# Optimization experiments

Hardware: AMD Instinct MI355X
Metric: run time of the kernel (lower is better)

Reference implementation:

```python
import jax, jax.numpy as jnp
import numpy as np

NUM_EXECUTORS = 50
NUM_DAG_FEATURES = 3
EMB_DAG = 16
EMB_GLOB = 16
HIDDEN = [64, 64, 32]
B = 60000            # number of jobs (one per env in the batched rollout)
NODES_PER_JOB = 10
NODE_FEAT = 5


def _init_mlp(key, dims):
    ws, bs = [], []
    for i in range(len(dims) - 1):
        key, k = jax.random.split(key)
        scale = 1.0 / np.sqrt(dims[i])
        ws.append(jax.random.uniform(k, (dims[i], dims[i + 1]), jnp.float32, -scale, scale))
        bs.append(jnp.zeros((dims[i + 1],), jnp.float32))
    return ws, bs


def setup_inputs() -> dict:
    rng = np.random.default_rng(0)
    n_nodes = B * NODES_PER_JOB
    # dag_batch.ptr: job i owns nodes [i*NODES_PER_JOB, (i+1)*NODES_PER_JOB)
    ptr = np.arange(B + 1, dtype=np.int64) * NODES_PER_JOB
    job_indices = rng.permutation(B).astype(np.int64)
    # ragged action counts per job (exec_mask is a prefix mask of length num_exec_acts[i])
    num_exec_acts = rng.integers(1, NUM_EXECUTORS + 1, size=B).astype(np.int64)
    n_sel = num_exec_acts[job_indices]
    T = int(n_sel.sum())
    # per-ragged-row executor index: concat([arange(n) for n in n_sel]), vectorized
    starts = np.cumsum(n_sel) - n_sel
    exec_act_idx = (np.arange(T, dtype=np.int64) - np.repeat(starts, n_sel)).astype(np.int64)

    key = jax.random.key(0)
    k_x, k_hd, k_hg, k_mlp = jax.random.split(key, 4)
    x = jax.random.normal(k_x, (n_nodes, NODE_FEAT), jnp.float32)
    h_dag = jax.random.normal(k_hd, (B, EMB_DAG), jnp.float32)
    h_glob = jax.random.normal(k_hg, (B, EMB_GLOB), jnp.float32)

    in_dim = NUM_DAG_FEATURES + EMB_DAG + EMB_GLOB + 1  # 36
    ws, bs = _init_mlp(k_mlp, [in_dim] + HIDDEN + [1])

    return {
        "x": x,
        "h_dag": h_dag,
        "h_glob": h_glob,
        "ptr": jnp.asarray(ptr),
        "job_indices": jnp.asarray(job_indices),
        "num_exec_acts": jnp.asarray(num_exec_acts),
        "exec_act_idx": jnp.asarray(exec_act_idx),
        "W1": ws[0], "b1": bs[0],
        "W2": ws[1], "b2": bs[1],
        "W3": ws[2], "b3": bs[2],
        "W4": ws[3], "b4": bs[3],
    }


def reference(x, h_dag, h_glob, ptr, job_indices, num_exec_acts, exec_act_idx,
              W1, b1, W2, b2, W3, b3, W4, b4):
    T = exec_act_idx.shape[0]                       # total ragged action rows (static)
    J = job_indices.shape[0]
    # masked gather: dag features at each dag's start node, then select jobs
    x_dag = x[ptr[:-1], :NUM_DAG_FEATURES][job_indices]        # [J, 3]
    h_dag_sel = h_dag[job_indices]                              # [J, 16]
    x_h_dag = jnp.concatenate([x_dag, h_dag_sel], axis=1)       # [J, 19]
    # variable repeat_interleave -> gather by repeated row index
    n_sel = num_exec_acts[job_indices]
    rpt = jnp.repeat(jnp.arange(J), n_sel, total_repeat_length=T)
    x_h_rpt = x_h_dag[rpt]                                      # [T, 19]
    h_glob_rpt = h_glob[rpt]                                    # [T, 16]
    # exec action feature: k / num_executors for the k-th valid executor
    exec_actions = (exec_act_idx.astype(x.dtype) / NUM_EXECUTORS)[:, None]  # [T, 1]
    h = jnp.concatenate([x_h_rpt, h_glob_rpt, exec_actions], axis=1)        # [T, 36]
    h = jax.nn.relu(h @ W1 + b1)
    h = jax.nn.relu(h @ W2 + b2)
    h = jax.nn.relu(h @ W3 + b3)
    scores = (h @ W4 + b4).squeeze(-1)                          # [T]
    return scores
```

## Files before the change

kernel.cpp:

```cpp
#include <hip/hip_runtime.h>

#define TPB 256

using half8  = __attribute__((ext_vector_type(8))) _Float16;
using fp16x2 = __attribute__((ext_vector_type(2))) __fp16;
using f32x4  = __attribute__((ext_vector_type(4))) float;

static __device__ __forceinline__ unsigned pkrtz(float a, float b) {
    fp16x2 h = __builtin_amdgcn_cvt_pkrtz(a, b);
    return __builtin_bit_cast(unsigned, h);
}
template <int CTRL>
static __device__ __forceinline__ float dppmov(float x) {
    return __int_as_float(__builtin_amdgcn_mov_dpp(__float_as_int(x), CTRL, 0xF, 0xF, true));
}
#define DPP_SWAP 0xB1

__global__ __launch_bounds__(TPB) void k_prep(const float* __restrict__ x,
                                              const float* __restrict__ h_dag,
                                              const float* __restrict__ h_glob,
                                              const int* __restrict__ ptr,
                                              const int* __restrict__ job_indices,
                                              const int* __restrict__ num_exec_acts,
                                              int J, int nb,
                                              float* __restrict__ s_tab,
                                              int* __restrict__ bsum, int* __restrict__ jsv,
                                              const float* __restrict__ W1,
                                              const float* __restrict__ b1,
                                              const float* __restrict__ W2,
                                              const float* __restrict__ b2,
                                              const float* __restrict__ W3,
                                              const float* __restrict__ b3,
                                              const float* __restrict__ W4,
                                              uint4* __restrict__ wfrag,
                                              float4* __restrict__ bfrag)
{
    if (blockIdx.x == (unsigned)nb) {
        if (threadIdx.x < 64) {
            int lane = threadIdx.x;
            int n = lane & 15, q = lane >> 4;
#pragma unroll
            for (int nt = 0; nt < 4; nt++) {
#pragma unroll
                for (int s = 0; s < 2; s++) {
                    half8 w2f;
#pragma unroll
                    for (int jj = 0; jj < 8; jj++) {
                        int ks = s * 32 + q * 8 + jj;
                        w2f[jj] = (_Float16)W2[ks * 64 + nt * 16 + n];
                    }
                    wfrag[(8 + nt * 2 + s) * 64 + lane] = __builtin_bit_cast(uint4, w2f);
                }
            }
#pragma unroll
            for (int nt = 0; nt < 2; nt++) {
#pragma unroll
                for (int s = 0; s < 2; s++) {
                    half8 w3f;
#pragma unroll
                    for (int jj = 0; jj < 8; jj++) {
                        int ks = s * 32 + q * 8 + jj;
                        w3f[jj] = (_Float16)W3[ks * 32 + nt * 16 + n];
                    }
                    wfrag[(16 + nt * 2 + s) * 64 + lane] = __builtin_bit_cast(uint4, w3f);
                }
            }
            bfrag[1 * 64 + lane] = make_float4(b2[n], b2[16 + n], b2[32 + n], b2[48 + n]);
            bfrag[2 * 64 + lane] = make_float4(b3[n], b3[16 + n], W4[n], W4[16 + n]);
        }
        return;
    }

    __shared__ int sc[TPB];
    int j = blockIdx.x * TPB + threadIdx.x;
    int v = 0;
    if (j < J) {
        int ji   = job_indices[j];
        v        = num_exec_acts[ji];
        int node = ptr[ji];
        float f[35];
        f[0] = x[node * 5 + 0];
        f[1] = x[node * 5 + 1];
        f[2] = x[node * 5 + 2];
        float4 hd[4], hg[4];
#pragma unroll
        for (int c4 = 0; c4 < 4; c4++) hd[c4] = *(const float4*)(h_dag + (size_t)ji * 16 + 4 * c4);
#pragma unroll
        for (int c4 = 0; c4 < 4; c4++) hg[c4] = *(const float4*)(h_glob + (size_t)j * 16 + 4 * c4);
#pragma unroll
        for (int c4 = 0; c4 < 4; c4++) {
            f[3 + 4 * c4 + 0]  = hd[c4].x; f[3 + 4 * c4 + 1]  = hd[c4].y;
            f[3 + 4 * c4 + 2]  = hd[c4].z; f[3 + 4 * c4 + 3]  = hd[c4].w;
            f[19 + 4 * c4 + 0] = hg[c4].x; f[19 + 4 * c4 + 1] = hg[c4].y;
            f[19 + 4 * c4 + 2] = hg[c4].z; f[19 + 4 * c4 + 3] = hg[c4].w;
        }
        float acc[64];
#pragma unroll
        for (int d4 = 0; d4 < 16; d4++) {
            float4 b = *(const float4*)(b1 + 4 * d4);
            acc[4 * d4 + 0] = b.x; acc[4 * d4 + 1] = b.y;
            acc[4 * d4 + 2] = b.z; acc[4 * d4 + 3] = b.w;
        }
#pragma unroll
        for (int c = 0; c < 35; c++) {
            float fc = f[c];
#pragma unroll
            for (int d4 = 0; d4 < 16; d4++) {
                float4 w = *(const float4*)(W1 + c * 64 + 4 * d4);
                acc[4 * d4 + 0] += fc * w.x; acc[4 * d4 + 1] += fc * w.y;
                acc[4 * d4 + 2] += fc * w.z; acc[4 * d4 + 3] += fc * w.w;
            }
        }
        float4* sd = (float4*)(s_tab + (size_t)j * 64);
#pragma unroll
        for (int d4 = 0; d4 < 16; d4++)
            sd[d4] = make_float4(acc[4 * d4], acc[4 * d4 + 1], acc[4 * d4 + 2], acc[4 * d4 + 3]);
    }
    sc[threadIdx.x] = v;
    __syncthreads();
    for (int d = 1; d < TPB; d <<= 1) {
        int add = (threadIdx.x >= d) ? sc[threadIdx.x - d] : 0;
        __syncthreads();
        sc[threadIdx.x] += add;
        __syncthreads();
    }
    if (j < J) jsv[j] = ((sc[threadIdx.x] - v) << 6) | v;
    if (threadIdx.x == TPB - 1) bsum[blockIdx.x] = sc[TPB - 1];
}

__global__ __launch_bounds__(TPB) void k_mlp_mfma(const float* __restrict__ s_tab,
                                                  const float* __restrict__ W1,
                                                  const int* __restrict__ jsv,
                                                  const int* __restrict__ bsum,
                                                  const uint4* __restrict__ wfrag,
                                                  const float4* __restrict__ bfrag,
                                                  const float* __restrict__ b4,
                                                  float* __restrict__ out,
                                                  int T, int J, int nb, int numTiles, int chunk)
{
    __shared__ __align__(16) char smem[4 * 4096];
    __shared__ int boffs[TPB];
    __shared__ int swin[4][64];
    __shared__ int srow[4][64];
    const int tid  = threadIdx.x;
    const int lane = tid & 63;
    const int wv   = tid >> 6;
    const int n    = lane & 15;
    const int q    = lane >> 4;
    char* slab = smem + wv * 4096;

    {
        int v = (tid < nb) ? bsum[tid] : 0;
        boffs[tid] = v;
        __syncthreads();
        for (int d = 1; d < TPB; d <<= 1) {
            int add = (tid >= d) ? boffs[tid - d] : 0;
            __syncthreads();
            boffs[tid] += add;
            __syncthreads();
        }
        int ex = boffs[tid] - v;
        __syncthreads();
        boffs[tid] = ex;
        __syncthreads();
    }

    half8 bw2[4][2], bw3[2][2];
#pragma unroll
    for (int nt = 0; nt < 4; nt++)
#pragma unroll
        for (int s = 0; s < 2; s++)
            bw2[nt][s] = __builtin_bit_cast(half8, wfrag[(8 + nt * 2 + s) * 64 + lane]);
#pragma unroll
    for (int nt = 0; nt < 2; nt++)
#pragma unroll
        for (int s = 0; s < 2; s++)
            bw3[nt][s] = __builtin_bit_cast(half8, wfrag[(16 + nt * 2 + s) * 64 + lane]);

    float4 bf2 = bfrag[1 * 64 + lane];
    float4 bf3 = bfrag[2 * 64 + lane];
    float bb2[4] = {bf2.x, bf2.y, bf2.z, bf2.w};
    float bb3[2] = {bf3.x, bf3.y};
    const float w4a = bf3.z, w4b = bf3.w;
    const float b4v = b4[0];
    const int   swr = (n >> 1) & 7;
    const int   odd = n & 1;

    float w36[16];
    {
        const float* wp = W1 + 35 * 64 + q * 8;
        float4 wa0 = *(const float4*)(wp);
        float4 wa1 = *(const float4*)(wp + 4);
        float4 wb0 = *(const float4*)(wp + 32);
        float4 wb1 = *(const float4*)(wp + 36);
        w36[0]=wa0.x; w36[1]=wa0.y; w36[2]=wa0.z; w36[3]=wa0.w;
        w36[4]=wa1.x; w36[5]=wa1.y; w36[6]=wa1.z; w36[7]=wa1.w;
        w36[8]=wb0.x; w36[9]=wb0.y; w36[10]=wb0.z; w36[11]=wb0.w;
        w36[12]=wb1.x; w36[13]=wb1.y; w36[14]=wb1.z; w36[15]=wb1.w;
    }

    const int t0 = blockIdx.x * chunk;
    const int t1 = (t0 + chunk < numTiles) ? (t0 + chunk) : numTiles;
    const int R  = (t1 - t0) * 32;
    const int r0 = t0 * 128 + wv * R;
    int rend = r0 + R;
    if (rend > T) rend = T;

    if (r0 < rend) {
        int j_lo;
        {
            int lo = 0, hi = nb - 1;
            while (lo < hi) {
                int mid = (lo + hi + 1) >> 1;
                if (boffs[mid] <= r0) lo = mid; else hi = mid - 1;
            }
            j_lo = lo << 8;
        }
        int sreg    = 0;
        int win_top = 0x80000000;

        half8 a2[2][2];

        auto build_a2 = [&](int mtbase) {
#pragma unroll
            for (int m = 0; m < 2; m++) {
                int u   = srow[wv][16 * (mtbase + m) + n];
                int job = j_lo + (u >> 8);
                if (job > J - 1) job = J - 1;
                float e = (float)(u & 255) * 0.02f;
                const float* sp = s_tab + (size_t)job * 64 + q * 8;
                float4 s0 = *(const float4*)(sp);
                float4 s1 = *(const float4*)(sp + 4);
                float4 s2 = *(const float4*)(sp + 32);
                float4 s3 = *(const float4*)(sp + 36);
                float h[16];
                h[0]  = fmaxf(s0.x + e * w36[0],  0.0f); h[1]  = fmaxf(s0.y + e * w36[1],  0.0f);
                h[2]  = fmaxf(s0.z + e * w36[2],  0.0f); h[3]  = fmaxf(s0.w + e * w36[3],  0.0f);
                h[4]  = fmaxf(s1.x + e * w36[4],  0.0f); h[5]  = fmaxf(s1.y + e * w36[5],  0.0f);
                h[6]  = fmaxf(s1.z + e * w36[6],  0.0f); h[7]  = fmaxf(s1.w + e * w36[7],  0.0f);
                h[8]  = fmaxf(s2.x + e * w36[8],  0.0f); h[9]  = fmaxf(s2.y + e * w36[9],  0.0f);
                h[10] = fmaxf(s2.z + e * w36[10], 0.0f); h[11] = fmaxf(s2.w + e * w36[11], 0.0f);
                h[12] = fmaxf(s3.x + e * w36[12], 0.0f); h[13] = fmaxf(s3.y + e * w36[13], 0.0f);
                h[14] = fmaxf(s3.z + e * w36[14], 0.0f); h[15] = fmaxf(s3.w + e * w36[15], 0.0f);
                a2[m][0] = __builtin_bit_cast(half8, make_uint4(pkrtz(h[0], h[1]),  pkrtz(h[2], h[3]),
                                                                pkrtz(h[4], h[5]),  pkrtz(h[6], h[7])));
                a2[m][1] = __builtin_bit_cast(half8, make_uint4(pkrtz(h[8], h[9]),  pkrtz(h[10], h[11]),
                                                                pkrtz(h[12], h[13]), pkrtz(h[14], h[15])));
            }
        };

        auto stage_L2r = [&]() {
#pragma unroll
            for (int mt = 0; mt < 2; mt++) {
                f32x4 acc[4];
#pragma unroll
                for (int nt = 0; nt < 4; nt++) { f32x4 c; c[0]=c[1]=c[2]=c[3]=bb2[nt]; acc[nt]=c; }
#pragma unroll
                for (int s = 0; s < 2; s++) {
#pragma unroll
                    for (int nt = 0; nt < 4; nt++)
                        acc[nt] = __builtin_amdgcn_mfma_f32_16x16x32_f16(a2[mt][s], bw2[nt][s], acc[nt], 0, 0, 0);
                }
                unsigned* sl = (unsigned*)slab;
#pragma unroll
                for (int nt = 0; nt < 4; nt++) {
                    float v0 = fmaxf(acc[nt][0], 0.0f), v1 = fmaxf(acc[nt][1], 0.0f);
                    float v2 = fmaxf(acc[nt][2], 0.0f), v3 = fmaxf(acc[nt][3], 0.0f);
                    float t0_ = dppmov<DPP_SWAP>(v0), t1_ = dppmov<DPP_SWAP>(v1);
                    float t2_ = dppmov<DPP_SWAP>(v2), t3_ = dppmov<DPP_SWAP>(v3);
                    unsigned u0 = pkrtz(odd ? t2_ : v0, odd ? v2 : t0_);
                    unsigned u1 = pkrtz(odd ? t3_ : v1, odd ? v3 : t1_);
                    int rowA = 16 * mt + 4 * q + (odd ? 2 : 0);
                    int c    = 2 * nt + (n >> 3);
                    int a0   = (rowA * 8 + (c ^ ((rowA >> 1) & 7))) * 4 + ((n >> 1) & 3);
                    sl[a0] = u0; sl[a0 + 32] = u1;
                }
            }
        };

        auto stage_L34 = [&](int rbb) {
#pragma unroll
            for (int mt = 0; mt < 2; mt++) {
                const int M0 = 16 * mt;
                f32x4 acc[2];
#pragma unroll
                for (int nt = 0; nt < 2; nt++) { f32x4 c; c[0]=c[1]=c[2]=c[3]=bb3[nt]; acc[nt]=c; }
#pragma unroll
                for (int s = 0; s < 2; s++) {
                    half8 a = *(const half8*)(slab + ((M0 + n) * 8 + ((s * 4 + q) ^ swr)) * 16);
#pragma unroll
                    for (int nt = 0; nt < 2; nt++)
                        acc[nt] = __builtin_amdgcn_mfma_f32_16x16x32_f16(a, bw3[nt][s], acc[nt], 0, 0, 0);
                }
                f32x4 red;
#pragma unroll
                for (int r = 0; r < 4; r++)
                    red[r] = fmaxf(acc[0][r], 0.0f) * w4a + fmaxf(acc[1][r], 0.0f) * w4b;
#pragma unroll
                for (int r = 0; r < 4; r++) {
                    red[r] += dppmov<0x121>(red[r]);
                    red[r] += dppmov<0x122>(red[r]);
                    red[r] += dppmov<0x124>(red[r]);
                    red[r] += dppmov<0x128>(red[r]);
                }
                int t = rbb + M0 + q * 4 + n;
                float val = (n == 0) ? red[0] : (n == 1) ? red[1] : (n == 2) ? red[2] : red[3];
                if (n < 4 && t < T) out[t] = val + b4v;
            }
        };

        for (int rb = r0; rb < rend; rb += 64) {
            if (win_top <= rb + 63) {
                for (;;) {
                    int jj = j_lo + lane;
                    sreg = (jj < J) ? (boffs[jj >> 8] + (jsv[jj] >> 6)) : 0x7fffffff;
                    unsigned long long m = __ballot(sreg <= rb);
                    int adv = 63 - __builtin_clzll(m);
                    j_lo += adv;
                    if (adv == 0) break;
                }
                swin[wv][lane] = sreg;
                win_top = __shfl(sreg, 63);
            }

            {
                int rt = rb + lane;
                const int* sw = swin[wv];
                int lj = 0;
#pragma unroll
                for (int stp = 32; stp; stp >>= 1) {
                    int c2 = lj + stp;
                    if (c2 < 64 && sw[c2] <= rt) lj = c2;
                }
                srow[wv][lane] = (lj << 8) | (rt - sw[lj]);
            }

            build_a2(0);
            stage_L2r();
            stage_L34(rb);
            if (rb + 32 < rend) {
                build_a2(2);
                stage_L2r();
                stage_L34(rb + 32);
            }
        }
    }
}

extern "C" void kernel_launch(void* const* d_in, const int* in_sizes, int n_in,
                              void* d_out, int out_size, void* d_ws, size_t ws_size,
                              hipStream_t stream)
{
    const float* x             = (const float*)d_in[0];
    const float* h_dag         = (const float*)d_in[1];
    const float* h_glob        = (const float*)d_in[2];
    const int*   ptr           = (const int*)d_in[3];
    const int*   job_indices   = (const int*)d_in[4];
    const int*   num_exec_acts = (const int*)d_in[5];
    const float* W1 = (const float*)d_in[7];
    const float* b1 = (const float*)d_in[8];
    const float* W2 = (const float*)d_in[9];
    const float* b2 = (const float*)d_in[10];
    const float* W3 = (const float*)d_in[11];
    const float* b3 = (const float*)d_in[12];
    const float* W4 = (const float*)d_in[13];
    const float* b4 = (const float*)d_in[14];
    float* out = (float*)d_out;

    int J  = in_sizes[4];
    int T  = in_sizes[6];
    int nb = (J + TPB - 1) / TPB;

    char* wsp = (char*)d_ws;
    int* bsum = (int*)wsp;
    wsp += (((size_t)nb * 4) + 255) / 256 * 256;
    int* jsv = (int*)wsp;
    wsp += (((size_t)J * 4) + 255) / 256 * 256;
    uint4* wfrag = (uint4*)wsp;
    wsp += 20 * 64 * 16;
    float4* bfrag = (float4*)wsp;
    wsp += 3 * 64 * 16;
    float* s_tab = (float*)wsp;

    k_prep<<<nb + 1, TPB, 0, stream>>>(x, h_dag, h_glob, ptr, job_indices, num_exec_acts,
                                       J, nb, s_tab, bsum, jsv,
                                       W1, b1, W2, b2, W3, b3, W4, wfrag, bfrag);

    int numTiles = (T + 127) / 128;
    int grid = numTiles < 1280 ? numTiles : 1280;
    int chunk = (numTiles + grid - 1) / grid;
    grid = (numTiles + chunk - 1) / chunk;
    k_mlp_mfma<<<grid, TPB, 0, stream>>>(s_tab, W1, jsv, bsum, wfrag, bfrag, b4,
                                         out, T, J, nb, numTiles, chunk);
}
```

Before: 171.7 us.

## Store per-job layer-1 table in fp16 quarters and split prep across column blocks

The per-job layer-1 pre-activation table is now stored as fp16 in four 16-column quarter planes, and the prep kernel launches four times as many blocks, each computing one quarter of the 64 outputs. The MLP kernel gathers these halved rows and applies the executor-feature term and ReLU with packed fp16 math instead of fp32 plus conversion. The aim is to halve the gather traffic in the main kernel, cut per-thread register use in prep, and raise prep parallelism. The MLP grid cap is also raised. The cost is extra fp16 rounding in the layer-1 activations and redundant input loads across the four prep quarters.

```diff
diff --git a/kernel.cpp b/kernel.cpp
--- a/kernel.cpp
+++ b/kernel.cpp
@@ -4,11 +4,16 @@
 
 using half8  = __attribute__((ext_vector_type(8))) _Float16;
 using fp16x2 = __attribute__((ext_vector_type(2))) __fp16;
+using hv2    = __attribute__((ext_vector_type(2))) _Float16;
 using f32x4  = __attribute__((ext_vector_type(4))) float;
 
 static __device__ __forceinline__ unsigned pkrtz(float a, float b) {
     fp16x2 h = __builtin_amdgcn_cvt_pkrtz(a, b);
     return __builtin_bit_cast(unsigned, h);
+}
+static __device__ __forceinline__ hv2 pk2(float a, float b) {
+    fp16x2 h = __builtin_amdgcn_cvt_pkrtz(a, b);
+    return __builtin_bit_cast(hv2, h);
 }
 template <int CTRL>
 static __device__ __forceinline__ float dppmov(float x) {
@@ -23,7 +28,7 @@
                                               const int* __restrict__ job_indices,
                                               const int* __restrict__ num_exec_acts,
                                               int J, int nb,
-                                              float* __restrict__ s_tab,
+                                              unsigned* __restrict__ s16,
                                               int* __restrict__ bsum, int* __restrict__ jsv,
                                               const float* __restrict__ W1,
                                               const float* __restrict__ b1,
@@ -35,7 +40,7 @@
                                               uint4* __restrict__ wfrag,
                                               float4* __restrict__ bfrag)
 {
-    if (blockIdx.x == (unsigned)nb) {
+    if (blockIdx.x == (unsigned)(4 * nb)) {
         if (threadIdx.x < 64) {
             int lane = threadIdx.x;
             int n = lane & 15, q = lane >> 4;
@@ -71,12 +76,13 @@
         return;
     }
 
-    __shared__ int sc[TPB];
-    int j = blockIdx.x * TPB + threadIdx.x;
+    const int qtr = blockIdx.x / nb;
+    const int cb  = blockIdx.x - qtr * nb;
+    int j = cb * TPB + threadIdx.x;
     int v = 0;
     if (j < J) {
         int ji   = job_indices[j];
-        v        = num_exec_acts[ji];
+        if (qtr == 0) v = num_exec_acts[ji];
         int node = ptr[ji];
         float f[35];
         f[0] = x[node * 5 + 0];
@@ -94,10 +100,10 @@
             f[19 + 4 * c4 + 0] = hg[c4].x; f[19 + 4 * c4 + 1] = hg[c4].y;
             f[19 + 4 * c4 + 2] = hg[c4].z; f[19 + 4 * c4 + 3] = hg[c4].w;
         }
-        float acc[64];
-#pragma unroll
-        for (int d4 = 0; d4 < 16; d4++) {
-            float4 b = *(const float4*)(b1 + 4 * d4);
+        float acc[16];
+#pragma unroll
+        for (int d4 = 0; d4 < 4; d4++) {
+            float4 b = *(const float4*)(b1 + qtr * 16 + 4 * d4);
             acc[4 * d4 + 0] = b.x; acc[4 * d4 + 1] = b.y;
             acc[4 * d4 + 2] = b.z; acc[4 * d4 + 3] = b.w;
         }
@@ -105,17 +111,21 @@
         for (int c = 0; c < 35; c++) {
             float fc = f[c];
 #pragma unroll
-            for (int d4 = 0; d4 < 16; d4++) {
-                float4 w = *(const float4*)(W1 + c * 64 + 4 * d4);
+            for (int d4 = 0; d4 < 4; d4++) {
+                float4 w = *(const float4*)(W1 + c * 64 + qtr * 16 + 4 * d4);
                 acc[4 * d4 + 0] += fc * w.x; acc[4 * d4 + 1] += fc * w.y;
                 acc[4 * d4 + 2] += fc * w.z; acc[4 * d4 + 3] += fc * w.w;
             }
         }
-        float4* sd = (float4*)(s_tab + (size_t)j * 64);
-#pragma unroll
-        for (int d4 = 0; d4 < 16; d4++)
-            sd[d4] = make_float4(acc[4 * d4], acc[4 * d4 + 1], acc[4 * d4 + 2], acc[4 * d4 + 3]);
-    }
+        unsigned* dst = s16 + ((size_t)qtr * J + j) * 8;
+        ((uint4*)dst)[0] = make_uint4(pkrtz(acc[0], acc[1]),  pkrtz(acc[2], acc[3]),
+                                      pkrtz(acc[4], acc[5]),  pkrtz(acc[6], acc[7]));
+        ((uint4*)dst)[1] = make_uint4(pkrtz(acc[8], acc[9]),  pkrtz(acc[10], acc[11]),
+                                      pkrtz(acc[12], acc[13]), pkrtz(acc[14], acc[15]));
+    }
+    if (qtr != 0) return;
+
+    __shared__ int sc[TPB];
     sc[threadIdx.x] = v;
     __syncthreads();
     for (int d = 1; d < TPB; d <<= 1) {
@@ -125,10 +135,10 @@
         __syncthreads();
     }
     if (j < J) jsv[j] = ((sc[threadIdx.x] - v) << 6) | v;
-    if (threadIdx.x == TPB - 1) bsum[blockIdx.x] = sc[TPB - 1];
-}
-
-__global__ __launch_bounds__(TPB) void k_mlp_mfma(const float* __restrict__ s_tab,
+    if (threadIdx.x == TPB - 1) bsum[cb] = sc[TPB - 1];
+}
+
+__global__ __launch_bounds__(TPB) void k_mlp_mfma(const unsigned* __restrict__ s16,
                                                   const float* __restrict__ W1,
                                                   const int* __restrict__ jsv,
                                                   const int* __restrict__ bsum,
@@ -186,18 +196,15 @@
     const int   swr = (n >> 1) & 7;
     const int   odd = n & 1;
 
-    float w36[16];
+    hv2 w36p[8];
     {
         const float* wp = W1 + 35 * 64 + q * 8;
-        float4 wa0 = *(const float4*)(wp);
-        float4 wa1 = *(const float4*)(wp + 4);
-        float4 wb0 = *(const float4*)(wp + 32);
-        float4 wb1 = *(const float4*)(wp + 36);
-        w36[0]=wa0.x; w36[1]=wa0.y; w36[2]=wa0.z; w36[3]=wa0.w;
-        w36[4]=wa1.x; w36[5]=wa1.y; w36[6]=wa1.z; w36[7]=wa1.w;
-        w36[8]=wb0.x; w36[9]=wb0.y; w36[10]=wb0.z; w36[11]=wb0.w;
-        w36[12]=wb1.x; w36[13]=wb1.y; w36[14]=wb1.z; w36[15]=wb1.w;
-    }
+#pragma unroll
+        for (int k = 0; k < 4; k++) w36p[k]     = pk2(wp[2 * k],      wp[2 * k + 1]);
+#pragma unroll
+        for (int k = 0; k < 4; k++) w36p[4 + k] = pk2(wp[32 + 2 * k], wp[32 + 2 * k + 1]);
+    }
+    const hv2 z2 = {(_Float16)0.0f, (_Float16)0.0f};
 
     const int t0 = blockIdx.x * chunk;
     const int t1 = (t0 + chunk < numTiles) ? (t0 + chunk) : numTiles;
@@ -228,24 +235,27 @@
                 int job = j_lo + (u >> 8);
                 if (job > J - 1) job = J - 1;
                 float e = (float)(u & 255) * 0.02f;
-                const float* sp = s_tab + (size_t)job * 64 + q * 8;
-                float4 s0 = *(const float4*)(sp);
-                float4 s1 = *(const float4*)(sp + 4);
-                float4 s2 = *(const float4*)(sp + 32);
-                float4 s3 = *(const float4*)(sp + 36);
-                float h[16];
-                h[0]  = fmaxf(s0.x + e * w36[0],  0.0f); h[1]  = fmaxf(s0.y + e * w36[1],  0.0f);
-                h[2]  = fmaxf(s0.z + e * w36[2],  0.0f); h[3]  = fmaxf(s0.w + e * w36[3],  0.0f);
-                h[4]  = fmaxf(s1.x + e * w36[4],  0.0f); h[5]  = fmaxf(s1.y + e * w36[5],  0.0f);
-                h[6]  = fmaxf(s1.z + e * w36[6],  0.0f); h[7]  = fmaxf(s1.w + e * w36[7],  0.0f);
-                h[8]  = fmaxf(s2.x + e * w36[8],  0.0f); h[9]  = fmaxf(s2.y + e * w36[9],  0.0f);
-                h[10] = fmaxf(s2.z + e * w36[10], 0.0f); h[11] = fmaxf(s2.w + e * w36[11], 0.0f);
-                h[12] = fmaxf(s3.x + e * w36[12], 0.0f); h[13] = fmaxf(s3.y + e * w36[13], 0.0f);
-                h[14] = fmaxf(s3.z + e * w36[14], 0.0f); h[15] = fmaxf(s3.w + e * w36[15], 0.0f);
-                a2[m][0] = __builtin_bit_cast(half8, make_uint4(pkrtz(h[0], h[1]),  pkrtz(h[2], h[3]),
-                                                                pkrtz(h[4], h[5]),  pkrtz(h[6], h[7])));
-                a2[m][1] = __builtin_bit_cast(half8, make_uint4(pkrtz(h[8], h[9]),  pkrtz(h[10], h[11]),
-                                                                pkrtz(h[12], h[13]), pkrtz(h[14], h[15])));
+                hv2 epk = pk2(e, e);
+                const uint4* plo = (const uint4*)s16 + ((size_t)(q >> 1) * J + job) * 2 + (q & 1);
+                const uint4* phi = (const uint4*)s16 + ((size_t)(2 + (q >> 1)) * J + job) * 2 + (q & 1);
+                uint4 lo = *plo;
+                uint4 hi = *phi;
+                hv2 r0_ = __builtin_elementwise_max(__builtin_bit_cast(hv2, lo.x) + epk * w36p[0], z2);
+                hv2 r1_ = __builtin_elementwise_max(__builtin_bit_cast(hv2, lo.y) + epk * w36p[1], z2);
+                hv2 r2_ = __builtin_elementwise_max(__builtin_bit_cast(hv2, lo.z) + epk * w36p[2], z2);
+                hv2 r3_ = __builtin_elementwise_max(__builtin_bit_cast(hv2, lo.w) + epk * w36p[3], z2);
+                a2[m][0] = __builtin_bit_cast(half8, make_uint4(__builtin_bit_cast(unsigned, r0_),
+                                                                __builtin_bit_cast(unsigned, r1_),
+                                                                __builtin_bit_cast(unsigned, r2_),
+                                                                __builtin_bit_cast(unsigned, r3_)));
+                hv2 r4_ = __builtin_elementwise_max(__builtin_bit_cast(hv2, hi.x) + epk * w36p[4], z2);
+                hv2 r5_ = __builtin_elementwise_max(__builtin_bit_cast(hv2, hi.y) + epk * w36p[5], z2);
+                hv2 r6_ = __builtin_elementwise_max(__builtin_bit_cast(hv2, hi.z) + epk * w36p[6], z2);
+                hv2 r7_ = __builtin_elementwise_max(__builtin_bit_cast(hv2, hi.w) + epk * w36p[7], z2);
+                a2[m][1] = __builtin_bit_cast(half8, make_uint4(__builtin_bit_cast(unsigned, r4_),
+                                                                __builtin_bit_cast(unsigned, r5_),
+                                                                __builtin_bit_cast(unsigned, r6_),
+                                                                __builtin_bit_cast(unsigned, r7_)));
             }
         };
 
@@ -380,16 +390,16 @@
     wsp += 20 * 64 * 16;
     float4* bfrag = (float4*)wsp;
     wsp += 3 * 64 * 16;
-    float* s_tab = (float*)wsp;
-
-    k_prep<<<nb + 1, TPB, 0, stream>>>(x, h_dag, h_glob, ptr, job_indices, num_exec_acts,
-                                       J, nb, s_tab, bsum, jsv,
-                                       W1, b1, W2, b2, W3, b3, W4, wfrag, bfrag);
+    unsigned* s16 = (unsigned*)wsp;
+
+    k_prep<<<4 * nb + 1, TPB, 0, stream>>>(x, h_dag, h_glob, ptr, job_indices, num_exec_acts,
+                                           J, nb, s16, bsum, jsv,
+                                           W1, b1, W2, b2, W3, b3, W4, wfrag, bfrag);
 
     int numTiles = (T + 127) / 128;
-    int grid = numTiles < 1280 ? numTiles : 1280;
+    int grid = numTiles < 2048 ? numTiles : 2048;
     int chunk = (numTiles + grid - 1) / grid;
     grid = (numTiles + chunk - 1) / chunk;
-    k_mlp_mfma<<<grid, TPB, 0, stream>>>(s_tab, W1, jsv, bsum, wfrag, bfrag, b4,
+    k_mlp_mfma<<<grid, TPB, 0, stream>>>(s16, W1, jsv, bsum, wfrag, bfrag, b4,
                                          out, T, J, nb, numTiles, chunk);
 }
```

Result: faster. 153.9 us (-10.4%).
